# Performance work log

Hardware: AMD Instinct MI355X
Metric: run time of the kernel (lower is better)

The kernel has to match this reference:

```python
import jax, jax.numpy as jnp
import numpy as np

SPARSITY_RATIO = 0.1


def setup_inputs() -> dict:
    key = jax.random.key(0)
    x = jax.random.normal(key, (4, 4096, 2048), dtype=jnp.float32)
    return {"x": x}


def reference(x):
    # x: [batch, seq_len, n_embd]
    B, S, D = x.shape
    k = max(1, int(D * SPARSITY_RATIO))
    # top-k by absolute value along the feature dim
    _, topk_idx = jax.lax.top_k(jnp.abs(x), k)  # [B, S, k]
    # scatter 1.0 at top-k positions (matches torch scatter_ mask construction)
    b = jnp.arange(B)[:, None, None]
    s = jnp.arange(S)[None, :, None]
    mask = jnp.zeros_like(x).at[b, s, topk_idx].set(1.0)
    scale = jnp.asarray(D / k, dtype=x.dtype)
    return x * mask * scale
```

## Files before the change

kernel.cpp:

```cpp
#include <hip/hip_runtime.h>


constexpr int D_DIM = 2048;
constexpr int K_SEL = 204;
constexpr int NT    = 256;
constexpr int RPW   = 2;

typedef float f32x4 __attribute__((ext_vector_type(4)));

__device__ __forceinline__ int dpp_reduce_add(int x) {
    x += __builtin_amdgcn_update_dpp(0, x, 0x111, 0xF, 0xF, true);
    x += __builtin_amdgcn_update_dpp(0, x, 0x112, 0xF, 0xF, true);
    x += __builtin_amdgcn_update_dpp(0, x, 0x114, 0xF, 0xF, true);
    x += __builtin_amdgcn_update_dpp(0, x, 0x118, 0xF, 0xF, true);
    x += __builtin_amdgcn_update_dpp(0, x, 0x142, 0xA, 0xF, false);
    x += __builtin_amdgcn_update_dpp(0, x, 0x143, 0xC, 0xF, false);
    return __builtin_amdgcn_readlane(x, 63);
}

__device__ __forceinline__ int wave_count_ge(const float4 (&f)[8], float t) {
    int c0 = 0, c1 = 0, c2 = 0, c3 = 0;
#pragma unroll
    for (int b = 0; b < 8; ++b) {
        c0 += (__builtin_fabsf(f[b].x) >= t) ? 1 : 0;
        c1 += (__builtin_fabsf(f[b].y) >= t) ? 1 : 0;
        c2 += (__builtin_fabsf(f[b].z) >= t) ? 1 : 0;
        c3 += (__builtin_fabsf(f[b].w) >= t) ? 1 : 0;
    }
    return dpp_reduce_add((c0 + c1) + (c2 + c3));
}

__device__ __forceinline__ void process_row(const float4 (&f)[8],
                                            float* __restrict__ outr,
                                            const int lane) {
    const float scale = 2048.0f / 204.0f;

    unsigned lo = 0u, hi = 0x80000000u;
    unsigned thr = 0u;
    bool done = false;

    {
        const int c = wave_count_ge(f, 1.6484375f);
        if (c == K_SEL) { thr = 0x3FD30000u; done = true; }
        else if (c > K_SEL) lo = 0x3FD30000u; else hi = 0x3FD30000u;
    }
    if (!done) {
        const unsigned p2 = (lo != 0u) ? 0x3FD60000u
                                       : 0x3FD00000u;
        const int c = wave_count_ge(f, __uint_as_float(p2));
        if (c == K_SEL) { thr = p2; done = true; }
        else if (c > K_SEL) lo = p2; else hi = p2;
    }
    if (!done) {
        unsigned p3 = 0u;
        if (hi == 0x80000000u)      p3 = 0x3FE00000u;
        else if (lo == 0u)          p3 = 0x3FC80000u;
        if (p3 != 0u) {
            const int c = wave_count_ge(f, __uint_as_float(p3));
            if (c == K_SEL) { thr = p3; done = true; }
            else if (c > K_SEL) lo = p3; else hi = p3;
        }
    }
    if (!done && lo == 0u) {
        const int c = wave_count_ge(f, 1.0f);
        if (c == K_SEL) { thr = 0x3F800000u; done = true; }
        else if (c > K_SEL) lo = 0x3F800000u; else hi = 0x3F800000u;
    }

#pragma unroll 1
    while (!done && (hi - lo) > 1u) {
        const unsigned mid = (lo + hi) >> 1;
        const int c = wave_count_ge(f, __uint_as_float(mid));
        if (c == K_SEL) { thr = mid; done = true; }
        else if (c > K_SEL) lo = mid; else hi = mid;
    }

    f32x4* op = reinterpret_cast<f32x4*>(outr);

    if (done) {
        const float tf = __uint_as_float(thr);
#pragma unroll
        for (int b = 0; b < 8; ++b) {
            f32x4 w;
            w.x = (__builtin_fabsf(f[b].x) >= tf) ? f[b].x * scale : 0.0f;
            w.y = (__builtin_fabsf(f[b].y) >= tf) ? f[b].y * scale : 0.0f;
            w.z = (__builtin_fabsf(f[b].z) >= tf) ? f[b].z * scale : 0.0f;
            w.w = (__builtin_fabsf(f[b].w) >= tf) ? f[b].w * scale : 0.0f;
            __builtin_nontemporal_store(w, op + b * 64 + lane);
        }
        return;
    }

    const float Tf = __uint_as_float(lo);
    int ge_pack = 0;
#pragma unroll
    for (int b = 0; b < 8; ++b) {
        ge_pack += (__builtin_fabsf(f[b].x) > Tf) ? 1 : 0;
        ge_pack += (__builtin_fabsf(f[b].y) > Tf) ? 1 : 0;
        ge_pack += (__builtin_fabsf(f[b].z) > Tf) ? 1 : 0;
        ge_pack += (__builtin_fabsf(f[b].w) > Tf) ? 1 : 0;
        ge_pack += (__builtin_fabsf(f[b].x) == Tf) ? (1 << 16) : 0;
        ge_pack += (__builtin_fabsf(f[b].y) == Tf) ? (1 << 16) : 0;
        ge_pack += (__builtin_fabsf(f[b].z) == Tf) ? (1 << 16) : 0;
        ge_pack += (__builtin_fabsf(f[b].w) == Tf) ? (1 << 16) : 0;
    }
    const int tot = dpp_reduce_add(ge_pack);
    const int cnt_gt = tot & 0xFFFF;
    const int neq = tot >> 16;
    const int r = K_SEL - cnt_gt;

    if (neq == r) {
#pragma unroll
        for (int b = 0; b < 8; ++b) {
            f32x4 w;
            w.x = (__builtin_fabsf(f[b].x) >= Tf) ? f[b].x * scale : 0.0f;
            w.y = (__builtin_fabsf(f[b].y) >= Tf) ? f[b].y * scale : 0.0f;
            w.z = (__builtin_fabsf(f[b].z) >= Tf) ? f[b].z * scale : 0.0f;
            w.w = (__builtin_fabsf(f[b].w) >= Tf) ? f[b].w * scale : 0.0f;
            __builtin_nontemporal_store(w, op + b * 64 + lane);
        }
        return;
    }

    const unsigned long long lt = (lane == 0) ? 0ull : (~0ull >> (64 - lane));
    int base = 0;
    for (int b = 0; b < 8; ++b) {
        const float fe[4] = { f[b].x, f[b].y, f[b].z, f[b].w };
        unsigned long long m[4];
#pragma unroll
        for (int e = 0; e < 4; ++e) m[e] = __ballot(__builtin_fabsf(fe[e]) == Tf);
        int cm = 0;
#pragma unroll
        for (int e = 0; e < 4; ++e) cm += __popcll(m[e] & lt);
        f32x4 w;
        float wv[4];
        int partial = 0;
#pragma unroll
        for (int e = 0; e < 4; ++e) {
            const int rank = base + cm + partial;
            const bool eq = (__builtin_fabsf(fe[e]) == Tf);
            const bool sel = (__builtin_fabsf(fe[e]) > Tf) || (eq && rank < r);
            wv[e] = sel ? fe[e] * scale : 0.0f;
            partial += (int)((m[e] >> lane) & 1ull);
        }
        w.x = wv[0]; w.y = wv[1]; w.z = wv[2]; w.w = wv[3];
        __builtin_nontemporal_store(w, op + b * 64 + lane);
#pragma unroll
        for (int e = 0; e < 4; ++e) base += __popcll(m[e]);
    }
}

__global__ __launch_bounds__(NT) void sparse_topk_kernel(const float* __restrict__ x,
                                                         float* __restrict__ out) {
    const int wave = threadIdx.x >> 6;
    const int lane = threadIdx.x & 63;
    const long long gw = (long long)blockIdx.x * 4 + wave;
    const long long r0 = gw * RPW;

    const float4* xp0 = reinterpret_cast<const float4*>(x + r0 * D_DIM);
    const float4* xp1 = reinterpret_cast<const float4*>(x + (r0 + 1) * D_DIM);

    float4 fA[8], fB[8];
#pragma unroll
    for (int b = 0; b < 8; ++b) fA[b] = xp0[b * 64 + lane];
#pragma unroll
    for (int b = 0; b < 8; ++b) fB[b] = xp1[b * 64 + lane];

    process_row(fA, out + r0 * D_DIM, lane);
    process_row(fB, out + (r0 + 1) * D_DIM, lane);
}

extern "C" void kernel_launch(void* const* d_in, const int* in_sizes, int n_in,
                              void* d_out, int out_size, void* d_ws, size_t ws_size,
                              hipStream_t stream) {
    const float* x = (const float*)d_in[0];
    float* out = (float*)d_out;
    const int rows = in_sizes[0] / D_DIM;
    sparse_topk_kernel<<<rows / (4 * RPW), NT, 0, stream>>>(x, out);
}
```

Baseline: 242.2 us.

## Process four rows per wave with double-buffered register prefetch

Each wave now handles four rows instead of two. It keeps two register buffers and loads the next row while the current row's threshold search runs, with sched_barriers keeping the issued loads from being reordered. This is meant to hide global load latency behind the compute. The trade-off is half as many blocks (fewer waves in flight) and extra register pressure from holding prefetched data during process_row.

```diff
diff --git a/kernel.cpp b/kernel.cpp
--- a/kernel.cpp
+++ b/kernel.cpp
@@ -4,7 +4,7 @@
 constexpr int D_DIM = 2048;
 constexpr int K_SEL = 204;
 constexpr int NT    = 256;
-constexpr int RPW   = 2;
+constexpr int RPW   = 4;
 
 typedef float f32x4 __attribute__((ext_vector_type(4)));
 
@@ -157,17 +157,41 @@
     const long long gw = (long long)blockIdx.x * 4 + wave;
     const long long r0 = gw * RPW;
 
-    const float4* xp0 = reinterpret_cast<const float4*>(x + r0 * D_DIM);
-    const float4* xp1 = reinterpret_cast<const float4*>(x + (r0 + 1) * D_DIM);
-
-    float4 fA[8], fB[8];
-#pragma unroll
-    for (int b = 0; b < 8; ++b) fA[b] = xp0[b * 64 + lane];
-#pragma unroll
-    for (int b = 0; b < 8; ++b) fB[b] = xp1[b * 64 + lane];
-
-    process_row(fA, out + r0 * D_DIM, lane);
-    process_row(fB, out + (r0 + 1) * D_DIM, lane);
+    const f32x4* xp = reinterpret_cast<const f32x4*>(x + r0 * D_DIM);
+    float* outr = out + r0 * D_DIM;
+
+    float4 A[8], B[8];
+
+#pragma unroll
+    for (int b = 0; b < 8; ++b) {
+        const f32x4 t = xp[b * 64 + lane];
+        A[b] = make_float4(t.x, t.y, t.z, t.w);
+    }
+#pragma unroll
+    for (int b = 0; b < 8; ++b) {
+        const f32x4 t = xp[512 + b * 64 + lane];
+        B[b] = make_float4(t.x, t.y, t.z, t.w);
+    }
+    __builtin_amdgcn_sched_barrier(0);
+
+    process_row(A, outr, lane);
+#pragma unroll
+    for (int b = 0; b < 8; ++b) {
+        const f32x4 t = xp[1024 + b * 64 + lane];
+        A[b] = make_float4(t.x, t.y, t.z, t.w);
+    }
+    __builtin_amdgcn_sched_barrier(0);
+
+    process_row(B, outr + D_DIM, lane);
+#pragma unroll
+    for (int b = 0; b < 8; ++b) {
+        const f32x4 t = xp[1536 + b * 64 + lane];
+        B[b] = make_float4(t.x, t.y, t.z, t.w);
+    }
+    __builtin_amdgcn_sched_barrier(0);
+
+    process_row(A, outr + 2 * D_DIM, lane);
+    process_row(B, outr + 3 * D_DIM, lane);
 }
 
 extern "C" void kernel_launch(void* const* d_in, const int* in_sizes, int n_in,
```

New measurement: 239.6 us. No clear change (-1.0%).

## Double-buffer row loads with explicit vmcnt waits, four rows per wave

Applied to the files above, without the earlier changes.

Each wave now handles four rows instead of two, using two register buffers. The next row's loads are issued with inline-asm global_load_dwordx4 while the current row's top-k threshold search runs, and explicit s_waitcnt vmcnt waits plus a sched_barrier control the ordering. The aim is to hide global-load latency behind the compute of the binary-search threshold. In exchange the grid has half as many blocks, which reduces parallelism. The hand-set vmcnt values also rely on in-order completion when loads are mixed with stores.

```diff
diff --git a/kernel.cpp b/kernel.cpp
--- a/kernel.cpp
+++ b/kernel.cpp
@@ -4,9 +4,21 @@
 constexpr int D_DIM = 2048;
 constexpr int K_SEL = 204;
 constexpr int NT    = 256;
-constexpr int RPW   = 2;
+constexpr int RPW   = 4;
 
 typedef float f32x4 __attribute__((ext_vector_type(4)));
+
+__device__ __forceinline__ f32x4 gload16(const f32x4* p) {
+    f32x4 r;
+    asm volatile("global_load_dwordx4 %0, %1, off" : "=v"(r) : "v"(p) : "memory");
+    return r;
+}
+
+#define VMWAIT(n)                                                  \
+    do {                                                           \
+        asm volatile("s_waitcnt vmcnt(" #n ")" ::: "memory");      \
+        __builtin_amdgcn_sched_barrier(0);                         \
+    } while (0)
 
 __device__ __forceinline__ int dpp_reduce_add(int x) {
     x += __builtin_amdgcn_update_dpp(0, x, 0x111, 0xF, 0xF, true);
@@ -18,7 +30,7 @@
     return __builtin_amdgcn_readlane(x, 63);
 }
 
-__device__ __forceinline__ int wave_count_ge(const float4 (&f)[8], float t) {
+__device__ __forceinline__ int wave_count_ge(const f32x4 (&f)[8], float t) {
     int c0 = 0, c1 = 0, c2 = 0, c3 = 0;
 #pragma unroll
     for (int b = 0; b < 8; ++b) {
@@ -30,7 +42,7 @@
     return dpp_reduce_add((c0 + c1) + (c2 + c3));
 }
 
-__device__ __forceinline__ void process_row(const float4 (&f)[8],
+__device__ __forceinline__ void process_row(const f32x4 (&f)[8],
                                             float* __restrict__ outr,
                                             const int lane) {
     const float scale = 2048.0f / 204.0f;
@@ -157,17 +169,31 @@
     const long long gw = (long long)blockIdx.x * 4 + wave;
     const long long r0 = gw * RPW;
 
-    const float4* xp0 = reinterpret_cast<const float4*>(x + r0 * D_DIM);
-    const float4* xp1 = reinterpret_cast<const float4*>(x + (r0 + 1) * D_DIM);
-
-    float4 fA[8], fB[8];
-#pragma unroll
-    for (int b = 0; b < 8; ++b) fA[b] = xp0[b * 64 + lane];
-#pragma unroll
-    for (int b = 0; b < 8; ++b) fB[b] = xp1[b * 64 + lane];
-
-    process_row(fA, out + r0 * D_DIM, lane);
-    process_row(fB, out + (r0 + 1) * D_DIM, lane);
+    const f32x4* xp = reinterpret_cast<const f32x4*>(x + r0 * D_DIM);
+    float* outr = out + r0 * D_DIM;
+
+    f32x4 A[8], B[8];
+
+#pragma unroll
+    for (int b = 0; b < 8; ++b) A[b] = gload16(xp + b * 64 + lane);
+#pragma unroll
+    for (int b = 0; b < 8; ++b) B[b] = gload16(xp + 512 + b * 64 + lane);
+
+    VMWAIT(8);
+    process_row(A, outr, lane);
+#pragma unroll
+    for (int b = 0; b < 8; ++b) A[b] = gload16(xp + 1024 + b * 64 + lane);
+
+    VMWAIT(16);
+    process_row(B, outr + D_DIM, lane);
+#pragma unroll
+    for (int b = 0; b < 8; ++b) B[b] = gload16(xp + 1536 + b * 64 + lane);
+
+    VMWAIT(16);
+    process_row(A, outr + 2 * D_DIM, lane);
+
+    VMWAIT(8);
+    process_row(B, outr + 3 * D_DIM, lane);
 }
 
 extern "C" void kernel_launch(void* const* d_in, const int* in_sizes, int n_in,
```

Result: faster. 236.1 us (-2.5%).

## Split top-k into threshold search kernel and streaming apply kernel

Applied to the files above, without the earlier changes.

The fused kernel is split in two. The first computes a per-row threshold, writing it to workspace and handling tie rows directly. The second is a grid-stride streaming kernel that re-reads x and writes the masked, scaled output. The aim is to decouple the latency-bound search from the bandwidth-bound write phase, at the cost of reading the input twice, adding a second launch, and dropping the two-rows-per-wave loading.

```diff
diff --git a/kernel.cpp b/kernel.cpp
--- a/kernel.cpp
+++ b/kernel.cpp
@@ -4,7 +4,6 @@
 constexpr int D_DIM = 2048;
 constexpr int K_SEL = 204;
 constexpr int NT    = 256;
-constexpr int RPW   = 2;
 
 typedef float f32x4 __attribute__((ext_vector_type(4)));
 
@@ -18,7 +17,7 @@
     return __builtin_amdgcn_readlane(x, 63);
 }
 
-__device__ __forceinline__ int wave_count_ge(const float4 (&f)[8], float t) {
+__device__ __forceinline__ int wave_count_ge(const f32x4 (&f)[8], float t) {
     int c0 = 0, c1 = 0, c2 = 0, c3 = 0;
 #pragma unroll
     for (int b = 0; b < 8; ++b) {
@@ -30,10 +29,17 @@
     return dpp_reduce_add((c0 + c1) + (c2 + c3));
 }
 
-__device__ __forceinline__ void process_row(const float4 (&f)[8],
-                                            float* __restrict__ outr,
-                                            const int lane) {
-    const float scale = 2048.0f / 204.0f;
+__global__ __launch_bounds__(NT) void thresh_kernel(const float* __restrict__ x,
+                                                    float* __restrict__ out,
+                                                    float* __restrict__ thrws) {
+    const int wave = threadIdx.x >> 6;
+    const int lane = threadIdx.x & 63;
+    const long long row = (long long)blockIdx.x * 4 + wave;
+
+    const f32x4* xp = reinterpret_cast<const f32x4*>(x + row * D_DIM);
+    f32x4 f[8];
+#pragma unroll
+    for (int b = 0; b < 8; ++b) f[b] = xp[b * 64 + lane];
 
     unsigned lo = 0u, hi = 0x80000000u;
     unsigned thr = 0u;
@@ -75,22 +81,12 @@
         else if (c > K_SEL) lo = mid; else hi = mid;
     }
 
-    f32x4* op = reinterpret_cast<f32x4*>(outr);
-
     if (done) {
-        const float tf = __uint_as_float(thr);
-#pragma unroll
-        for (int b = 0; b < 8; ++b) {
-            f32x4 w;
-            w.x = (__builtin_fabsf(f[b].x) >= tf) ? f[b].x * scale : 0.0f;
-            w.y = (__builtin_fabsf(f[b].y) >= tf) ? f[b].y * scale : 0.0f;
-            w.z = (__builtin_fabsf(f[b].z) >= tf) ? f[b].z * scale : 0.0f;
-            w.w = (__builtin_fabsf(f[b].w) >= tf) ? f[b].w * scale : 0.0f;
-            __builtin_nontemporal_store(w, op + b * 64 + lane);
-        }
+        if (lane == 0) thrws[row] = __uint_as_float(thr);
         return;
     }
 
+    const float scale = 2048.0f / 204.0f;
     const float Tf = __uint_as_float(lo);
     int ge_pack = 0;
 #pragma unroll
@@ -106,22 +102,9 @@
     }
     const int tot = dpp_reduce_add(ge_pack);
     const int cnt_gt = tot & 0xFFFF;
-    const int neq = tot >> 16;
     const int r = K_SEL - cnt_gt;
 
-    if (neq == r) {
-#pragma unroll
-        for (int b = 0; b < 8; ++b) {
-            f32x4 w;
-            w.x = (__builtin_fabsf(f[b].x) >= Tf) ? f[b].x * scale : 0.0f;
-            w.y = (__builtin_fabsf(f[b].y) >= Tf) ? f[b].y * scale : 0.0f;
-            w.z = (__builtin_fabsf(f[b].z) >= Tf) ? f[b].z * scale : 0.0f;
-            w.w = (__builtin_fabsf(f[b].w) >= Tf) ? f[b].w * scale : 0.0f;
-            __builtin_nontemporal_store(w, op + b * 64 + lane);
-        }
-        return;
-    }
-
+    f32x4* op = reinterpret_cast<f32x4*>(out + row * D_DIM);
     const unsigned long long lt = (lane == 0) ? 0ull : (~0ull >> (64 - lane));
     int base = 0;
     for (int b = 0; b < 8; ++b) {
@@ -148,26 +131,33 @@
 #pragma unroll
         for (int e = 0; e < 4; ++e) base += __popcll(m[e]);
     }
+    if (lane == 0) thrws[row] = __uint_as_float(0xFF800000u);
 }
 
-__global__ __launch_bounds__(NT) void sparse_topk_kernel(const float* __restrict__ x,
-                                                         float* __restrict__ out) {
-    const int wave = threadIdx.x >> 6;
-    const int lane = threadIdx.x & 63;
-    const long long gw = (long long)blockIdx.x * 4 + wave;
-    const long long r0 = gw * RPW;
+constexpr int AP_BLOCKS = 2048;
 
-    const float4* xp0 = reinterpret_cast<const float4*>(x + r0 * D_DIM);
-    const float4* xp1 = reinterpret_cast<const float4*>(x + (r0 + 1) * D_DIM);
-
-    float4 fA[8], fB[8];
-#pragma unroll
-    for (int b = 0; b < 8; ++b) fA[b] = xp0[b * 64 + lane];
-#pragma unroll
-    for (int b = 0; b < 8; ++b) fB[b] = xp1[b * 64 + lane];
-
-    process_row(fA, out + r0 * D_DIM, lane);
-    process_row(fB, out + (r0 + 1) * D_DIM, lane);
+__global__ __launch_bounds__(NT) void apply_kernel(const float* __restrict__ x,
+                                                   const float* __restrict__ thrws,
+                                                   float* __restrict__ out,
+                                                   long long n4) {
+    const float scale = 2048.0f / 204.0f;
+    const f32x4* xp = reinterpret_cast<const f32x4*>(x);
+    f32x4* op = reinterpret_cast<f32x4*>(out);
+    long long i = (long long)blockIdx.x * NT + threadIdx.x;
+    const long long stride = (long long)AP_BLOCKS * NT;
+#pragma unroll 4
+    for (; i < n4; i += stride) {
+        const int row = (int)(i >> 9);
+        const float thr = thrws[row];
+        const f32x4 v = xp[i];
+        if (thr < 0.0f) continue;
+        f32x4 w;
+        w.x = (__builtin_fabsf(v.x) >= thr) ? v.x * scale : 0.0f;
+        w.y = (__builtin_fabsf(v.y) >= thr) ? v.y * scale : 0.0f;
+        w.z = (__builtin_fabsf(v.z) >= thr) ? v.z * scale : 0.0f;
+        w.w = (__builtin_fabsf(v.w) >= thr) ? v.w * scale : 0.0f;
+        __builtin_nontemporal_store(w, op + i);
+    }
 }
 
 extern "C" void kernel_launch(void* const* d_in, const int* in_sizes, int n_in,
@@ -175,6 +165,10 @@
                               hipStream_t stream) {
     const float* x = (const float*)d_in[0];
     float* out = (float*)d_out;
+    float* thrws = (float*)d_ws;
     const int rows = in_sizes[0] / D_DIM;
-    sparse_topk_kernel<<<rows / (4 * RPW), NT, 0, stream>>>(x, out);
+    const long long n4 = (long long)rows * (D_DIM / 4);
+
+    thresh_kernel<<<rows / 4, NT, 0, stream>>>(x, out, thrws);
+    apply_kernel<<<AP_BLOCKS, NT, 0, stream>>>(x, thrws, out, n4);
 }
```

Result: no change. 246.5 us (+1.8%).
